# Kernel optimization log

Measured on AMD Instinct MI355X. Metric: run time of the kernel, lower is better.

## Reference

```python
import jax, jax.numpy as jnp
import numpy as np

G = 16                 # grid side -> 4096 voxels
N_GRID = G ** 3
N_NODES = 4096         # protein nodes
DEG = 256              # node neighbors per grid voxel
HID = 64               # MPNN hidden == ResNet in_channels
NUM_CLASSES = 20
BN = np.float32(1.0 / np.sqrt(1.0 + 1e-5))  # eval-mode BatchNorm3d (mean=0, var=1, gamma=1, beta=0)


def _lin(key, fi, fo):
    return jax.random.normal(key, (fi, fo), jnp.float32) * (fi ** -0.5)


def _cw(key, o, i, k):
    return jax.random.normal(key, (o, i, k, k, k), jnp.float32) * ((i * k ** 3) ** -0.5)


def setup_inputs() -> dict:
    key = jax.random.key(0)
    ks = jax.random.split(key, 32)
    n_edges = N_GRID * DEG
    # every grid voxel receives exactly DEG messages (bincount never zero)
    edge_i = jax.random.randint(ks[0], (n_edges,), 0, N_NODES, dtype=jnp.int32)
    edge_j = jnp.repeat(jnp.arange(N_GRID, dtype=jnp.int32), DEG)
    edge_index = jnp.stack([edge_i, edge_j])  # [2, E]

    node_embedding = jax.random.normal(ks[1], (N_NODES, HID), jnp.float32)
    node_pos = jax.random.uniform(ks[2], (N_NODES, 3), jnp.float32)
    gx = (jnp.arange(G, dtype=jnp.float32) + 0.5) / G
    gd, gh, gw = jnp.meshgrid(gx, gx, gx, indexing='ij')
    grid_pos = jnp.stack([gd, gh, gw], -1).reshape(N_GRID, 3)

    z = lambda n: jnp.zeros((n,), jnp.float32)
    return {
        'node_embedding': node_embedding, 'node_pos': node_pos,
        'grid_pos': grid_pos, 'edge_index': edge_index,
        # MPNN edge / message / update MLPs
        'ew1': _lin(ks[3], 6, HID), 'eb1': z(HID), 'ew2': _lin(ks[4], HID, HID), 'eb2': z(HID),
        'mw1': _lin(ks[5], 2 * HID, HID), 'mb1': z(HID), 'mw2': _lin(ks[6], HID, HID), 'mb2': z(HID),
        'uw1': _lin(ks[7], HID, HID), 'ub1': z(HID), 'uw2': _lin(ks[8], HID, HID), 'ub2': z(HID),
        # ResNet3D: 3 Blocks (conv3 a, conv3 b, conv5 shortcut) with channels 64->64, 64->128, 128->256
        'c1a': _cw(ks[9], 64, 64, 3), 'c1b': _cw(ks[10], 64, 64, 3), 'c1s': _cw(ks[11], 64, 64, 5),
        'c2a': _cw(ks[12], 128, 64, 3), 'c2b': _cw(ks[13], 128, 128, 3), 'c2s': _cw(ks[14], 128, 64, 5),
        'c3a': _cw(ks[15], 256, 128, 3), 'c3b': _cw(ks[16], 256, 256, 3), 'c3s': _cw(ks[17], 256, 128, 5),
        'fcw': _lin(ks[18], 256, NUM_CLASSES), 'fcb': z(NUM_CLASSES),
    }


def _mlp(x, w1, b1, w2, b2):
    return jax.nn.silu(x @ w1 + b1) @ w2 + b2


def _conv(x, w, p):
    return jax.lax.conv_general_dilated(
        x, w, window_strides=(1, 1, 1), padding=[(p, p)] * 3,
        dimension_numbers=('NCDHW', 'OIDHW', 'NCDHW'))


def _block(x, wa, wb, ws):
    out = jax.nn.relu(_conv(x, wa, 1) * BN)
    out = _conv(out, wb, 1) * BN
    sc = _conv(x, ws, 2) * BN
    return jax.nn.relu(out + sc)


def reference(node_embedding, node_pos, grid_pos, edge_index,
              ew1, eb1, ew2, eb2, mw1, mb1, mw2, mb2, uw1, ub1, uw2, ub2,
              c1a, c1b, c1s, c2a, c2b, c2s, c3a, c3b, c3s, fcw, fcb):
    i, j = edge_index[0], edge_index[1]
    # ---- MPNN: gather, edge MLP, message MLP, scatter-mean, update MLP ----
    edge_attr = jnp.concatenate([node_pos[i], grid_pos[j]], axis=-1)        # [E, 6]
    pos_emb = _mlp(edge_attr, ew1, eb1, ew2, eb2)                           # [E, H]
    msg = _mlp(jnp.concatenate([node_embedding[i], pos_emb], -1),
               mw1, mb1, mw2, mb2)                                          # [E, H]
    agg = jax.ops.segment_sum(msg, j, num_segments=N_GRID)                  # [N_GRID, H]
    cnt = jax.ops.segment_sum(jnp.ones((msg.shape[0],), msg.dtype), j,
                              num_segments=N_GRID)
    grid_feat = _mlp(agg / cnt[:, None], uw1, ub1, uw2, ub2)                # [N_GRID, H]
    # ---- ResNet3D over the grid volume ----
    x = grid_feat.T.reshape(1, HID, G, G, G) * BN                           # instance_norm1 (eval BN)
    x = _block(x, c1a, c1b, c1s)
    x = _block(x, c2a, c2b, c2s)
    x = _block(x, c3a, c3b, c3s)
    pooled = jnp.max(x, axis=(2, 3, 4))                                     # max_pool3d(kernel=spatial)
    return pooled @ fcw + fcb                                               # [1, NUM_CLASSES]
```

## Files before the change

### kernel.cpp

```cpp
#include <hip/hip_runtime.h>
#include <math.h>

#define BN_S 0.9999950000374997f

typedef _Float16 half8 __attribute__((ext_vector_type(8)));
typedef float f32x4 __attribute__((ext_vector_type(4)));

__device__ __forceinline__ float silu_f(float x) {
    return __fdividef(x, 1.0f + __expf(-x));
}

__device__ __forceinline__ void gld16(const void* g, void* l) {
    __builtin_amdgcn_global_load_lds(
        (const __attribute__((address_space(1))) void*)g,
        (__attribute__((address_space(3))) void*)l, 16, 0, 0);
}

__global__ __launch_bounds__(64) void prep_w_k(
    const float* __restrict__ ew2, const float* __restrict__ mw1,
    const float* __restrict__ mw2, const float* __restrict__ uw1,
    const float* __restrict__ mb2, const float* __restrict__ ub1,
    float* __restrict__ W_mu, float* __restrict__ b_mu,
    _Float16* __restrict__ wemt_h, _Float16* __restrict__ wemt_l)
{
    const int k = blockIdx.x, c = threadIdx.x;
    float s = 0.f;
    for (int m = 0; m < 64; m++) s = fmaf(ew2[k*64 + m], mw1[(64 + m)*64 + c], s);
    {
        const int q = k >> 5, kg = (k >> 3) & 3, jj = k & 7;
        const int sl = q*256 + c*4 + kg;
        const int p = sl ^ ((sl >> 3) & 7);
        const _Float16 h = (_Float16)s;
        const _Float16 l = (_Float16)(s - (float)h);
        wemt_h[p*8 + jj] = h;
        wemt_l[p*8 + jj] = l;
    }
    float s2 = 0.f;
    for (int m = 0; m < 64; m++) s2 = fmaf(mw2[k*64 + m], uw1[m*64 + c], s2);
    W_mu[k*64 + c] = s2;
    if (k == 0) {
        float s3 = ub1[c];
        for (int m = 0; m < 64; m++) s3 = fmaf(mb2[m], uw1[m*64 + c], s3);
        b_mu[c] = s3;
    }
}

__global__ __launch_bounds__(64) void prep_nodes_k(
    const float* __restrict__ node_embedding, const float* __restrict__ node_pos,
    const float* __restrict__ grid_pos, const float* __restrict__ ew1,
    const float* __restrict__ eb1, const float* __restrict__ mw1,
    const float* __restrict__ mb1, const float* __restrict__ eb2,
    float* __restrict__ a_node, float* __restrict__ g_vox, float* __restrict__ n_node)
{
    const int v = blockIdx.x, c = threadIdx.x;
    const float p0 = node_pos[v*3], p1 = node_pos[v*3 + 1], p2 = node_pos[v*3 + 2];
    a_node[v*64 + c] = fmaf(p0, ew1[c], fmaf(p1, ew1[64 + c], fmaf(p2, ew1[128 + c], eb1[c])));
    const float q0 = grid_pos[v*3], q1 = grid_pos[v*3 + 1], q2 = grid_pos[v*3 + 2];
    g_vox[v*64 + c] = fmaf(q0, ew1[192 + c], fmaf(q1, ew1[256 + c], q2 * ew1[320 + c]));
    float s = mb1[c];
    for (int k = 0; k < 64; k++) s = fmaf(node_embedding[v*64 + k], mw1[k*64 + c], s);
    for (int k = 0; k < 64; k++) s = fmaf(eb2[k], mw1[(64 + k)*64 + c], s);
    n_node[v*64 + c] = s;
}

template<int K3, int NCOG, int NCH>
__global__ __launch_bounds__(256) void wsplit_k(
    const float* __restrict__ w, _Float16* __restrict__ dh, _Float16* __restrict__ dl,
    int CI)
{
    __shared__ float s[32*K3];
    const int co = blockIdx.x, cig = blockIdx.y, t = threadIdx.x;
    const float* src = w + ((size_t)co*CI + cig*32)*K3;
    for (int m = t; m < 32*K3; m += 256) s[m] = src[m];
    __syncthreads();
    const int coG = co >> 6, col = co & 63;
    for (int m = t; m < 32*K3; m += 256) {
        const int tap = m >> 5, cil = m & 31;
        const float x = s[cil*K3 + tap];
        const _Float16 h = (_Float16)x;
        const _Float16 l = (_Float16)(x - (float)h);
        const int b = cil >> 3, jj = cil & 7;
        const int sl = col*4 + b;
        const int p = sl ^ ((sl >> 3) & 7);
        const size_t base = ((size_t)(tap*NCOG + coG)*NCH + cig) * 2048;
        dh[base + p*8 + jj] = h;
        dl[base + p*8 + jj] = l;
    }
}

__global__ __launch_bounds__(256, 3) void edge_kernel(
    const int* __restrict__ edge_i,
    const float* __restrict__ a_node, const float* __restrict__ g_vox,
    const float* __restrict__ n_node,
    const _Float16* __restrict__ wemt_h, const _Float16* __restrict__ wemt_l,
    const float* __restrict__ W_mu, const float* __restrict__ b_mu,
    const float* __restrict__ uw2, const float* __restrict__ ub2,
    _Float16* __restrict__ x0h, _Float16* __restrict__ x0l)
{
    __shared__ __align__(16) _Float16 sAh[4096], sAl[4096];
    __shared__ __align__(16) _Float16 sBh[4096], sBl[4096];
    __shared__ float sV1[64], sV2[64], sRed[4*64];

    const int j = blockIdx.x, t = threadIdx.x;
    const int lane = t & 63, wv = t >> 6, ln15 = lane & 15, kg = lane >> 4;
    const int ebase = j << 8;

    gld16(wemt_h + t*8, &sAh[t*8]);
    gld16(wemt_h + 2048 + t*8, &sAh[2048 + t*8]);
    gld16(wemt_l + t*8, &sAl[t*8]);
    gld16(wemt_l + 2048 + t*8, &sAl[2048 + t*8]);

    const int r = t >> 2, sub = t & 3;
    float4 gv4[4];
    #pragma unroll
    for (int m4 = 0; m4 < 4; m4++)
        gv4[m4] = *(const float4*)&g_vox[j*64 + sub*16 + m4*4];

    float4 A[2][4], N[2][4];
    {
        const int iA = edge_i[ebase + r];
        #pragma unroll
        for (int m4 = 0; m4 < 4; m4++)
            A[0][m4] = *(const float4*)&a_node[(size_t)iA*64 + sub*16 + m4*4];
        #pragma unroll
        for (int eF = 0; eF < 4; eF++) {
            const int ieX = edge_i[ebase + eF*16 + ln15];
            N[0][eF] = *(const float4*)&n_node[(size_t)ieX*64 + wv*16 + kg*4];
        }
    }

    asm volatile("s_waitcnt vmcnt(0)" ::: "memory");
    __syncthreads();

    float psum[4] = {0.f, 0.f, 0.f, 0.f};

    #pragma unroll
    for (int T = 0; T < 4; T++) {
        const int par = T & 1;
        {
            float s1[16];
            #pragma unroll
            for (int m4 = 0; m4 < 4; m4++) {
                const float4 a = A[par][m4], g = gv4[m4];
                s1[m4*4 + 0] = silu_f(a.x + g.x);
                s1[m4*4 + 1] = silu_f(a.y + g.y);
                s1[m4*4 + 2] = silu_f(a.z + g.z);
                s1[m4*4 + 3] = silu_f(a.w + g.w);
            }
            half8 h0, l0, h1, l1;
            #pragma unroll
            for (int m = 0; m < 8; m++) {
                h0[m] = (_Float16)s1[m];
                l0[m] = (_Float16)(s1[m] - (float)h0[m]);
                h1[m] = (_Float16)s1[8 + m];
                l1[m] = (_Float16)(s1[8 + m] - (float)h1[m]);
            }
            const int q = sub >> 1, kg0 = (sub & 1) * 2;
            const int slot0 = (q*4 + kg0)*64 + r;
            *(half8*)&sBh[slot0*8] = h0; *(half8*)&sBl[slot0*8] = l0;
            *(half8*)&sBh[(slot0 + 64)*8] = h1; *(half8*)&sBl[(slot0 + 64)*8] = l1;
        }
        if (T < 3) {
            const int b1 = ebase + (T + 1)*64;
            const int iA = edge_i[b1 + r];
            #pragma unroll
            for (int m4 = 0; m4 < 4; m4++)
                A[par ^ 1][m4] = *(const float4*)&a_node[(size_t)iA*64 + sub*16 + m4*4];
            #pragma unroll
            for (int eF = 0; eF < 4; eF++) {
                const int ieX = edge_i[b1 + eF*16 + ln15];
                N[par ^ 1][eF] = *(const float4*)&n_node[(size_t)ieX*64 + wv*16 + kg*4];
            }
        }
        __syncthreads();
        #pragma unroll
        for (int eF = 0; eF < 4; eF++) {
            const int e = eF*16 + ln15;
            f32x4 acc;
            {
                const float4 nv = N[par][eF];
                acc[0] = nv.x; acc[1] = nv.y; acc[2] = nv.z; acc[3] = nv.w;
            }
            #pragma unroll
            for (int q = 0; q < 2; q++) {
                const int sa = q*256 + (wv*16 + ln15)*4 + kg;
                const int pa = sa ^ ((sa >> 3) & 7);
                const half8 Ah = *(const half8*)&sAh[pa*8];
                const half8 Al = *(const half8*)&sAl[pa*8];
                const int sb = ((q*4 + kg)*64 + e)*8;
                const half8 Bh = *(const half8*)&sBh[sb];
                const half8 Bl = *(const half8*)&sBl[sb];
                acc = __builtin_amdgcn_mfma_f32_16x16x32_f16(Ah, Bh, acc, 0, 0, 0);
                acc = __builtin_amdgcn_mfma_f32_16x16x32_f16(Ah, Bl, acc, 0, 0, 0);
                acc = __builtin_amdgcn_mfma_f32_16x16x32_f16(Al, Bh, acc, 0, 0, 0);
            }
            #pragma unroll
            for (int rg = 0; rg < 4; rg++) psum[rg] += silu_f(acc[rg]);
        }
        __syncthreads();
    }

    #pragma unroll
    for (int rg = 0; rg < 4; rg++) {
        float v = psum[rg];
        v += __shfl_xor(v, 1, 64); v += __shfl_xor(v, 2, 64);
        v += __shfl_xor(v, 4, 64); v += __shfl_xor(v, 8, 64);
        psum[rg] = v;
    }
    if (ln15 == 0) {
        #pragma unroll
        for (int rg = 0; rg < 4; rg++)
            sV1[wv*16 + kg*4 + rg] = psum[rg] * (1.0f / 256.0f);
    }
    __syncthreads();
    {
        const int c = t & 63, part = t >> 6;
        float h = (part == 0) ? b_mu[c] : 0.f;
        #pragma unroll
        for (int k2 = 0; k2 < 16; k2++) {
            const int k = part*16 + k2;
            h = fmaf(sV1[k], W_mu[k*64 + c], h);
        }
        sRed[part*64 + c] = h;
    }
    __syncthreads();
    if (t < 64)
        sV2[t] = silu_f(sRed[t] + sRed[64 + t] + sRed[128 + t] + sRed[192 + t]);
    __syncthreads();
    {
        const int c = t & 63, part = t >> 6;
        float g = (part == 0) ? ub2[c] : 0.f;
        #pragma unroll
        for (int k2 = 0; k2 < 16; k2++) {
            const int k = part*16 + k2;
            g = fmaf(sV2[k], uw2[k*64 + c], g);
        }
        sRed[part*64 + c] = g;
    }
    __syncthreads();
    if (t < 64) {
        const float val = (sRed[t] + sRed[64 + t] + sRed[128 + t] + sRed[192 + t]) * BN_S;
        const _Float16 hh = (_Float16)val;
        const _Float16 ll = (_Float16)(val - (float)hh);
        const int c = t, zz = j >> 8, v = j & 255;
        const int oct = (c >> 3) & 3;
        const int vsw = v ^ (oct << 1);
        const size_t a16 = ((size_t)((c >> 5)*16 + zz)*1024 + oct*256 + vsw)*8 + (c & 7);
        x0h[a16] = hh; x0l[a16] = ll;
    }
}

template<int KK, int CI, int NCO32, int CIS>
__global__ __launch_bounds__(256, 4) void conv_mfma_k(
    const _Float16* __restrict__ xh, const _Float16* __restrict__ xl,
    const _Float16* __restrict__ wh, const _Float16* __restrict__ wl,
    float* __restrict__ slab)
{
    constexpr int P = KK/2, K2 = KK*KK, NCH = CI/32, NCHS = NCH/CIS;
    constexpr int CO = NCO32*32, NCOG64 = NCO32/2;
    const int d0 = blockIdx.x, coG32 = blockIdx.y;
    const int co64G = coG32 >> 1, coHalf = coG32 & 1;
    const int cis = blockIdx.z / KK, kd = blockIdx.z % KK;
    const int t = threadIdx.x;
    const int lane = t & 63, wv = t >> 6;
    const int ln15 = lane & 15, kg = lane >> 4;

    float* sout = slab + ((size_t)blockIdx.z*CO + coG32*32)*4096 + d0*256;
    const int z = d0 + kd - P;
    if ((unsigned)z >= 16u) {
        for (int m = t; m < 32*256; m += 256)
            sout[(size_t)(m >> 8)*4096 + (m & 255)] = 0.f;
        return;
    }

    __shared__ __align__(16) _Float16 sXh[8192];
    __shared__ __align__(16) _Float16 sXl[8192];
    __shared__ __align__(16) _Float16 zb[8];
    if (t < 8) zb[t] = (_Float16)0.f;

    int aoff[2];
    #pragma unroll
    for (int cf = 0; cf < 2; cf++) {
        const int s = (coHalf*32 + cf*16 + ln15)*4 + kg;
        aoff[cf] = (s ^ ((s >> 3) & 7)) * 8;
    }

    auto stage_X = [&](int ch) {
        const size_t b16 = ((size_t)ch*16 + z) * 8192;
        #pragma unroll
        for (int q = 0; q < 4; q++) {
            gld16(xh + b16 + (q*256 + t)*8, &sXh[(q*256 + t)*8]);
            gld16(xl + b16 + (q*256 + t)*8, &sXl[(q*256 + t)*8]);
        }
    };
    auto loadA = [&](int ch, int t2, half8* Ah, half8* Al) {
        const size_t b = ((size_t)((kd*K2 + t2)*NCOG64 + co64G)*NCH + ch) * 2048;
        #pragma unroll
        for (int cf = 0; cf < 2; cf++) {
            Ah[cf] = *(const half8*)&wh[b + aoff[cf]];
            Al[cf] = *(const half8*)&wl[b + aoff[cf]];
        }
    };

    f32x4 acc[2][4];
    #pragma unroll
    for (int a = 0; a < 2; a++)
        #pragma unroll
        for (int b = 0; b < 4; b++)
            #pragma unroll
            for (int r2 = 0; r2 < 4; r2++) acc[a][b][r2] = 0.f;

    const int ch0 = cis * NCHS;
    half8 nAh[2], nAl[2];
    stage_X(ch0);
    loadA(ch0, 0, nAh, nAl);
    asm volatile("s_waitcnt vmcnt(0)" ::: "memory");
    __syncthreads();

    for (int cc = 0; cc < NCHS; cc++) {
        const int ch = ch0 + cc;
        for (int t2 = 0; t2 < K2; t2++) {
            half8 cAh[2], cAl[2];
            #pragma unroll
            for (int cf = 0; cf < 2; cf++) { cAh[cf] = nAh[cf]; cAl[cf] = nAl[cf]; }
            if (t2 + 1 < K2)          loadA(ch, t2 + 1, nAh, nAl);
            else if (cc + 1 < NCHS)   loadA(ch + 1, 0, nAh, nAl);

            const int kh = t2 / KK, kw = t2 % KK;
            __builtin_amdgcn_s_setprio(1);
            #pragma unroll
            for (int f = 0; f < 4; f++) {
                const int h_in = wv*4 + f + kh - P;
                if ((unsigned)h_in < 16u) {
                    const int w_in = ln15 + kw - P;
                    const bool ok = (unsigned)w_in < 16u;
                    const int slot = ok ? (kg*256 + h_in*16 + (w_in ^ (kg << 1))) : 0;
                    const half8 Bh = ok ? *(const half8*)&sXh[slot*8] : *(const half8*)zb;
                    const half8 Bl = ok ? *(const half8*)&sXl[slot*8] : *(const half8*)zb;
                    #pragma unroll
                    for (int cf = 0; cf < 2; cf++) {
                        acc[cf][f] = __builtin_amdgcn_mfma_f32_16x16x32_f16(cAh[cf], Bh, acc[cf][f], 0, 0, 0);
                        acc[cf][f] = __builtin_amdgcn_mfma_f32_16x16x32_f16(cAh[cf], Bl, acc[cf][f], 0, 0, 0);
                        acc[cf][f] = __builtin_amdgcn_mfma_f32_16x16x32_f16(cAl[cf], Bh, acc[cf][f], 0, 0, 0);
                    }
                }
            }
            __builtin_amdgcn_s_setprio(0);
        }
        if (cc + 1 < NCHS) {
            __syncthreads();
            stage_X(ch + 1);
            asm volatile("s_waitcnt vmcnt(0)" ::: "memory");
            __syncthreads();
        }
    }

    #pragma unroll
    for (int cf = 0; cf < 2; cf++)
        #pragma unroll
        for (int f = 0; f < 4; f++)
            #pragma unroll
            for (int r2 = 0; r2 < 4; r2++)
                sout[(size_t)(cf*16 + kg*4 + r2)*4096 + wv*64 + f*16 + ln15] = acc[cf][f][r2];
}

template<int S, int RMODE, int OUT>
__global__ __launch_bounds__(256) void reduce_k(
    const float* __restrict__ pbuf, const float* __restrict__ addsrc,
    float* __restrict__ outf, _Float16* __restrict__ oh, _Float16* __restrict__ ol,
    int CO)
{
    const int z = blockIdx.x, c8 = blockIdx.y, v = threadIdx.x;
    float val[8];
    #pragma unroll
    for (int jj = 0; jj < 8; jj++) {
        const int c = c8*8 + jj;
        float a = 0.f;
        #pragma unroll
        for (int s = 0; s < S; s++)
            a += pbuf[((size_t)s*CO + c)*4096 + z*256 + v];
        a *= BN_S;
        if (RMODE == 3) a += addsrc[(size_t)c*4096 + z*256 + v];
        if (RMODE != 2) a = fmaxf(a, 0.f);
        val[jj] = a;
    }
    if (OUT == 0) {
        #pragma unroll
        for (int jj = 0; jj < 8; jj++)
            outf[(size_t)(c8*8 + jj)*4096 + z*256 + v] = val[jj];
    } else if (OUT == 1) {
        half8 hv, lv;
        #pragma unroll
        for (int jj = 0; jj < 8; jj++) {
            hv[jj] = (_Float16)val[jj];
            lv[jj] = (_Float16)(val[jj] - (float)hv[jj]);
        }
        const int oct = c8 & 3;
        const int vsw = v ^ (oct << 1);
        const size_t a16 = ((size_t)((c8 >> 2)*16 + z)*1024 + oct*256 + vsw)*8;
        *(half8*)&oh[a16] = hv;
        *(half8*)&ol[a16] = lv;
    } else {
        __shared__ float sm[4][8];
        #pragma unroll
        for (int jj = 0; jj < 8; jj++) {
            float m = val[jj];
            m = fmaxf(m, __shfl_xor(m, 1, 64));  m = fmaxf(m, __shfl_xor(m, 2, 64));
            m = fmaxf(m, __shfl_xor(m, 4, 64));  m = fmaxf(m, __shfl_xor(m, 8, 64));
            m = fmaxf(m, __shfl_xor(m, 16, 64)); m = fmaxf(m, __shfl_xor(m, 32, 64));
            if ((v & 63) == 0) sm[v >> 6][jj] = m;
        }
        __syncthreads();
        if (v < 8) {
            const float m = fmaxf(fmaxf(sm[0][v], sm[1][v]), fmaxf(sm[2][v], sm[3][v]));
            outf[z*CO + c8*8 + v] = m;
        }
    }
}

__global__ __launch_bounds__(256) void fc_k(
    const float* __restrict__ pp, const float* __restrict__ fcw,
    const float* __restrict__ fcb, float* __restrict__ out)
{
    __shared__ float sp[256];
    const int t = threadIdx.x;
    float m = pp[t];
    for (int zz = 1; zz < 16; zz++) m = fmaxf(m, pp[zz*256 + t]);
    sp[t] = m;
    __syncthreads();
    if (t < 20) {
        float s = fcb[t];
        for (int c = 0; c < 256; c++) s = fmaf(sp[c], fcw[c*20 + t], s);
        out[t] = s;
    }
}

extern "C" void kernel_launch(void* const* d_in, const int* in_sizes, int n_in,
                              void* d_out, int out_size, void* d_ws, size_t ws_size,
                              hipStream_t stream)
{
    const float* node_embedding = (const float*)d_in[0];
    const float* node_pos       = (const float*)d_in[1];
    const float* grid_pos       = (const float*)d_in[2];
    const int*   edge_index     = (const int*)d_in[3];
    const float* ew1 = (const float*)d_in[4];
    const float* eb1 = (const float*)d_in[5];
    const float* ew2 = (const float*)d_in[6];
    const float* eb2 = (const float*)d_in[7];
    const float* mw1 = (const float*)d_in[8];
    const float* mb1 = (const float*)d_in[9];
    const float* mw2 = (const float*)d_in[10];
    const float* mb2 = (const float*)d_in[11];
    const float* uw1 = (const float*)d_in[12];
    const float* ub1 = (const float*)d_in[13];
    const float* uw2 = (const float*)d_in[14];
    const float* ub2 = (const float*)d_in[15];
    const float* c1a = (const float*)d_in[16];
    const float* c1b = (const float*)d_in[17];
    const float* c1s = (const float*)d_in[18];
    const float* c2a = (const float*)d_in[19];
    const float* c2b = (const float*)d_in[20];
    const float* c2s = (const float*)d_in[21];
    const float* c3a = (const float*)d_in[22];
    const float* c3b = (const float*)d_in[23];
    const float* c3s = (const float*)d_in[24];
    const float* fcw = (const float*)d_in[25];
    const float* fcb = (const float*)d_in[26];
    float* out = (float*)d_out;
    const int* edge_i = edge_index;

    float* ws = (float*)d_ws;
    float* a_node = ws;                ws += 262144;
    float* g_vox  = ws;                ws += 262144;
    float* n_node = ws;                ws += 262144;
    float* W_mu   = ws;                ws += 4096;
    float* b_mu   = ws;                ws += 64;
    _Float16* wemt_h = (_Float16*)ws;  ws += 2048;
    _Float16* wemt_l = (_Float16*)ws;  ws += 2048;
    _Float16* x0h = (_Float16*)ws;     ws += 131072;
    _Float16* x0l = (_Float16*)ws;     ws += 131072;
    _Float16* t2h = (_Float16*)ws;     ws += 262144;
    _Float16* t2l = (_Float16*)ws;     ws += 262144;
    _Float16* x2h = (_Float16*)ws;     ws += 262144;
    _Float16* x2l = (_Float16*)ws;     ws += 262144;
    _Float16* t3h = (_Float16*)ws;     ws += 524288;
    _Float16* t3l = (_Float16*)ws;     ws += 524288;
    float* u2 = ws;                    ws += 524288;
    float* u3 = ws;                    ws += 1048576;
    float* slab = ws;                  ws += 5242880;
    float* poolPart = ws;              ws += 4096;
    _Float16* wh = (_Float16*)ws;      ws += 4585472;
    _Float16* wl = (_Float16*)ws;      ws += 4585472;
    _Float16* t1h = (_Float16*)a_node;
    _Float16* t1l = (_Float16*)(a_node + 131072);
    float* u1 = g_vox;
    _Float16* x1h = (_Float16*)n_node;
    _Float16* x1l = (_Float16*)(n_node + 131072);

    _Float16* w1a_h = wh + 0;       _Float16* w1a_l = wl + 0;
    _Float16* w1b_h = wh + 110592;  _Float16* w1b_l = wl + 110592;
    _Float16* w1s_h = wh + 221184;  _Float16* w1s_l = wl + 221184;
    _Float16* w2a_h = wh + 733184;  _Float16* w2a_l = wl + 733184;
    _Float16* w2b_h = wh + 954368;  _Float16* w2b_l = wl + 954368;
    _Float16* w2s_h = wh + 1396736; _Float16* w2s_l = wl + 1396736;
    _Float16* w3a_h = wh + 2420736; _Float16* w3a_l = wl + 2420736;
    _Float16* w3b_h = wh + 3305472; _Float16* w3b_l = wl + 3305472;
    _Float16* w3s_h = wh + 5074944; _Float16* w3s_l = wl + 5074944;

    hipLaunchKernelGGL((wsplit_k<27,1,2>),  dim3(64,2),  dim3(256), 0, stream, c1a, w1a_h, w1a_l, 64);
    hipLaunchKernelGGL((wsplit_k<27,1,2>),  dim3(64,2),  dim3(256), 0, stream, c1b, w1b_h, w1b_l, 64);
    hipLaunchKernelGGL((wsplit_k<125,1,2>), dim3(64,2),  dim3(256), 0, stream, c1s, w1s_h, w1s_l, 64);
    hipLaunchKernelGGL((wsplit_k<27,2,2>),  dim3(128,2), dim3(256), 0, stream, c2a, w2a_h, w2a_l, 64);
    hipLaunchKernelGGL((wsplit_k<27,2,4>),  dim3(128,4), dim3(256), 0, stream, c2b, w2b_h, w2b_l, 128);
    hipLaunchKernelGGL((wsplit_k<125,2,2>), dim3(128,2), dim3(256), 0, stream, c2s, w2s_h, w2s_l, 64);
    hipLaunchKernelGGL((wsplit_k<27,4,4>),  dim3(256,4), dim3(256), 0, stream, c3a, w3a_h, w3a_l, 128);
    hipLaunchKernelGGL((wsplit_k<27,4,8>),  dim3(256,8), dim3(256), 0, stream, c3b, w3b_h, w3b_l, 256);
    hipLaunchKernelGGL((wsplit_k<125,4,4>), dim3(256,4), dim3(256), 0, stream, c3s, w3s_h, w3s_l, 128);

    hipLaunchKernelGGL(prep_w_k, dim3(64), dim3(64), 0, stream,
                       ew2, mw1, mw2, uw1, mb2, ub1, W_mu, b_mu, wemt_h, wemt_l);
    hipLaunchKernelGGL(prep_nodes_k, dim3(4096), dim3(64), 0, stream,
                       node_embedding, node_pos, grid_pos, ew1, eb1, mw1, mb1, eb2,
                       a_node, g_vox, n_node);
    hipLaunchKernelGGL(edge_kernel, dim3(4096), dim3(256), 0, stream,
                       edge_i, a_node, g_vox, n_node, wemt_h, wemt_l,
                       W_mu, b_mu, uw2, ub2, x0h, x0l);

    hipLaunchKernelGGL((conv_mfma_k<3,64,2,2>), dim3(16,2,6), dim3(256), 0, stream, x0h, x0l, w1a_h, w1a_l, slab);
    hipLaunchKernelGGL((reduce_k<6,1,1>), dim3(16,8), dim3(256), 0, stream, slab, (const float*)nullptr, (float*)nullptr, t1h, t1l, 64);
    hipLaunchKernelGGL((conv_mfma_k<3,64,2,2>), dim3(16,2,6), dim3(256), 0, stream, t1h, t1l, w1b_h, w1b_l, slab);
    hipLaunchKernelGGL((reduce_k<6,2,0>), dim3(16,8), dim3(256), 0, stream, slab, (const float*)nullptr, u1, (_Float16*)nullptr, (_Float16*)nullptr, 64);
    hipLaunchKernelGGL((conv_mfma_k<5,64,2,2>), dim3(16,2,10), dim3(256), 0, stream, x0h, x0l, w1s_h, w1s_l, slab);
    hipLaunchKernelGGL((reduce_k<10,3,1>), dim3(16,8), dim3(256), 0, stream, slab, u1, (float*)nullptr, x1h, x1l, 64);
    hipLaunchKernelGGL((conv_mfma_k<3,64,4,2>), dim3(16,4,6), dim3(256), 0, stream, x1h, x1l, w2a_h, w2a_l, slab);
    hipLaunchKernelGGL((reduce_k<6,1,1>), dim3(16,16), dim3(256), 0, stream, slab, (const float*)nullptr, (float*)nullptr, t2h, t2l, 128);
    hipLaunchKernelGGL((conv_mfma_k<3,128,4,2>), dim3(16,4,6), dim3(256), 0, stream, t2h, t2l, w2b_h, w2b_l, slab);
    hipLaunchKernelGGL((reduce_k<6,2,0>), dim3(16,16), dim3(256), 0, stream, slab, (const float*)nullptr, u2, (_Float16*)nullptr, (_Float16*)nullptr, 128);
    hipLaunchKernelGGL((conv_mfma_k<5,64,4,2>), dim3(16,4,10), dim3(256), 0, stream, x1h, x1l, w2s_h, w2s_l, slab);
    hipLaunchKernelGGL((reduce_k<10,3,1>), dim3(16,16), dim3(256), 0, stream, slab, u2, (float*)nullptr, x2h, x2l, 128);
    hipLaunchKernelGGL((conv_mfma_k<3,128,8,1>), dim3(16,8,3), dim3(256), 0, stream, x2h, x2l, w3a_h, w3a_l, slab);
    hipLaunchKernelGGL((reduce_k<3,1,1>), dim3(16,32), dim3(256), 0, stream, slab, (const float*)nullptr, (float*)nullptr, t3h, t3l, 256);
    hipLaunchKernelGGL((conv_mfma_k<3,256,8,1>), dim3(16,8,3), dim3(256), 0, stream, t3h, t3l, w3b_h, w3b_l, slab);
    hipLaunchKernelGGL((reduce_k<3,2,0>), dim3(16,32), dim3(256), 0, stream, slab, (const float*)nullptr, u3, (_Float16*)nullptr, (_Float16*)nullptr, 256);
    hipLaunchKernelGGL((conv_mfma_k<5,128,8,1>), dim3(16,8,5), dim3(256), 0, stream, x2h, x2l, w3s_h, w3s_l, slab);
    hipLaunchKernelGGL((reduce_k<5,3,2>), dim3(16,32), dim3(256), 0, stream, slab, u3, poolPart, (_Float16*)nullptr, (_Float16*)nullptr, 256);

    hipLaunchKernelGGL(fc_k, dim3(1), dim3(256), 0, stream, poolPart, fcw, fcb, out);

    (void)in_sizes; (void)n_in; (void)out_size; (void)ws_size;
}
```

Baseline: 540.5 us.

## Double-buffer edge B tile, swizzle LDS slots, pack fp16 conversions

The edge kernel's B-operand shared buffers are doubled so that each iteration writes the alternate buffer, which removes the trailing barrier per iteration (one sync per tile instead of two). LDS slot indices for the B tile get an XOR swizzle to reduce bank conflicts on the writes and MFMA reads. The hi/lo fp16 split now uses packed round-toward-zero conversion instead of per-element round-to-nearest casts. This doubles B-tile LDS usage, which may affect occupancy, and changes the rounding of the hi/lo split slightly.

New measurement: 535.8 us. About the same (-0.9%).

```diff
diff --git a/kernel.cpp b/kernel.cpp
--- a/kernel.cpp
+++ b/kernel.cpp
@@ -98,7 +98,7 @@
     _Float16* __restrict__ x0h, _Float16* __restrict__ x0l)
 {
     __shared__ __align__(16) _Float16 sAh[4096], sAl[4096];
-    __shared__ __align__(16) _Float16 sBh[4096], sBl[4096];
+    __shared__ __align__(16) _Float16 sBh[2][4096], sBl[2][4096];
     __shared__ float sV1[64], sV2[64], sRed[4*64];
 
     const int j = blockIdx.x, t = threadIdx.x;
@@ -138,27 +138,38 @@
     for (int T = 0; T < 4; T++) {
         const int par = T & 1;
         {
-            float s1[16];
+            float s1v[16];
             #pragma unroll
             for (int m4 = 0; m4 < 4; m4++) {
                 const float4 a = A[par][m4], g = gv4[m4];
-                s1[m4*4 + 0] = silu_f(a.x + g.x);
-                s1[m4*4 + 1] = silu_f(a.y + g.y);
-                s1[m4*4 + 2] = silu_f(a.z + g.z);
-                s1[m4*4 + 3] = silu_f(a.w + g.w);
+                s1v[m4*4 + 0] = silu_f(a.x + g.x);
+                s1v[m4*4 + 1] = silu_f(a.y + g.y);
+                s1v[m4*4 + 2] = silu_f(a.z + g.z);
+                s1v[m4*4 + 3] = silu_f(a.w + g.w);
             }
-            half8 h0, l0, h1, l1;
+            uint32_t hw[8], lw[8];
             #pragma unroll
             for (int m = 0; m < 8; m++) {
-                h0[m] = (_Float16)s1[m];
-                l0[m] = (_Float16)(s1[m] - (float)h0[m]);
-                h1[m] = (_Float16)s1[8 + m];
-                l1[m] = (_Float16)(s1[8 + m] - (float)h1[m]);
+                const auto hp = __builtin_amdgcn_cvt_pkrtz(s1v[2*m], s1v[2*m + 1]);
+                const float h0f = (float)hp[0], h1f = (float)hp[1];
+                const auto lp = __builtin_amdgcn_cvt_pkrtz(s1v[2*m] - h0f, s1v[2*m + 1] - h1f);
+                hw[m] = __builtin_bit_cast(uint32_t, hp);
+                lw[m] = __builtin_bit_cast(uint32_t, lp);
             }
             const int q = sub >> 1, kg0 = (sub & 1) * 2;
-            const int slot0 = (q*4 + kg0)*64 + r;
-            *(half8*)&sBh[slot0*8] = h0; *(half8*)&sBl[slot0*8] = l0;
-            *(half8*)&sBh[(slot0 + 64)*8] = h1; *(half8*)&sBl[(slot0 + 64)*8] = l1;
+            const int sl0 = (q*4 + kg0)*64 + r;
+            const int sl1 = sl0 + 64;
+            const int p0 = sl0 ^ ((sl0 >> 6) & 7);
+            const int p1 = sl1 ^ ((sl1 >> 6) & 7);
+            uint4 u;
+            u.x = hw[0]; u.y = hw[1]; u.z = hw[2]; u.w = hw[3];
+            *(uint4*)&sBh[par][p0*8] = u;
+            u.x = hw[4]; u.y = hw[5]; u.z = hw[6]; u.w = hw[7];
+            *(uint4*)&sBh[par][p1*8] = u;
+            u.x = lw[0]; u.y = lw[1]; u.z = lw[2]; u.w = lw[3];
+            *(uint4*)&sBl[par][p0*8] = u;
+            u.x = lw[4]; u.y = lw[5]; u.z = lw[6]; u.w = lw[7];
+            *(uint4*)&sBl[par][p1*8] = u;
         }
         if (T < 3) {
             const int b1 = ebase + (T + 1)*64;
@@ -182,14 +193,15 @@
                 acc[0] = nv.x; acc[1] = nv.y; acc[2] = nv.z; acc[3] = nv.w;
             }
             #pragma unroll
-            for (int q = 0; q < 2; q++) {
-                const int sa = q*256 + (wv*16 + ln15)*4 + kg;
+            for (int q2 = 0; q2 < 2; q2++) {
+                const int sa = q2*256 + (wv*16 + ln15)*4 + kg;
                 const int pa = sa ^ ((sa >> 3) & 7);
                 const half8 Ah = *(const half8*)&sAh[pa*8];
                 const half8 Al = *(const half8*)&sAl[pa*8];
-                const int sb = ((q*4 + kg)*64 + e)*8;
-                const half8 Bh = *(const half8*)&sBh[sb];
-                const half8 Bl = *(const half8*)&sBl[sb];
+                const int sbs = (q2*4 + kg)*64 + e;
+                const int pb = sbs ^ ((sbs >> 6) & 7);
+                const half8 Bh = *(const half8*)&sBh[par][pb*8];
+                const half8 Bl = *(const half8*)&sBl[par][pb*8];
                 acc = __builtin_amdgcn_mfma_f32_16x16x32_f16(Ah, Bh, acc, 0, 0, 0);
                 acc = __builtin_amdgcn_mfma_f32_16x16x32_f16(Ah, Bl, acc, 0, 0, 0);
                 acc = __builtin_amdgcn_mfma_f32_16x16x32_f16(Al, Bh, acc, 0, 0, 0);
@@ -197,7 +209,6 @@
             #pragma unroll
             for (int rg = 0; rg < 4; rg++) psum[rg] += silu_f(acc[rg]);
         }
-        __syncthreads();
     }
 
     #pragma unroll
@@ -207,6 +218,7 @@
         v += __shfl_xor(v, 4, 64); v += __shfl_xor(v, 8, 64);
         psum[rg] = v;
     }
+    __syncthreads();
     if (ln15 == 0) {
         #pragma unroll
         for (int rg = 0; rg < 4; rg++)
```
